# Optimization experiments

Measured on AMD Instinct MI355X. Metric: run time of the kernel, lower is better.

The kernel has to match this reference:

```python
import jax, jax.numpy as jnp
import numpy as np

N_NODES = 100000


def _gcn_conv(x, edge_index, W, b, n_nodes):
    """PyG GCNConv: add self-loops, symmetric deg^-1/2 normalization,
    linear transform, scatter-sum aggregation, bias."""
    loop = jnp.arange(n_nodes, dtype=edge_index.dtype)
    src = jnp.concatenate([edge_index[0], loop])  # message sources
    dst = jnp.concatenate([edge_index[1], loop])  # message targets
    deg = jax.ops.segment_sum(jnp.ones_like(dst, dtype=x.dtype), dst,
                              num_segments=n_nodes)
    dinv = jnp.where(deg > 0, jax.lax.rsqrt(jnp.maximum(deg, 1.0)), 0.0)
    norm = dinv[src] * dinv[dst]  # [E+N]
    h = x @ W  # [N, out] transform before aggregation (fewer bytes moved)
    msg = h[src] * norm[:, None]  # [E+N, out]
    out = jax.ops.segment_sum(msg, dst, num_segments=n_nodes)
    return out + b


def setup_inputs() -> dict:
    key = jax.random.key(0)
    k1, k2, k3, k4, k5, k6 = jax.random.split(key, 6)
    in_ch, hid, out_ch = 128, 64, 64
    x = jax.random.normal(k1, (N_NODES, in_ch), dtype=jnp.float32)
    edge_index = jax.random.randint(k2, (2, 3200000), 0, N_NODES, dtype=jnp.int64)
    # Glorot-style init for GCN weights, zeros for bias (PyG default)
    W1 = jax.random.normal(k3, (in_ch, hid), dtype=jnp.float32) / np.sqrt(in_ch)
    b1 = jnp.zeros((hid,), dtype=jnp.float32)
    W2 = jax.random.normal(k4, (hid, out_ch), dtype=jnp.float32) / np.sqrt(hid)
    b2 = jnp.zeros((out_ch,), dtype=jnp.float32)
    return {"x": x, "edge_index": edge_index, "W1": W1, "b1": b1,
            "W2": W2, "b2": b2}


def reference(x, edge_index, W1, b1, W2, b2):
    n = x.shape[0]
    h = _gcn_conv(x, edge_index, W1, b1, n)
    h = jax.nn.relu(h)
    out = _gcn_conv(h, edge_index, W2, b2, n)
    return out
```

## Files before the change

kernel.cpp:

```cpp
#include <hip/hip_runtime.h>
#include <math.h>


#define BKT_SHIFT 9
#define BKT_NODES 512
#define NBSH      256
#define CHUNK     8192
#define MAXB      20480

typedef unsigned short ushort_t;

static __device__ __forceinline__ unsigned short f2bf(float f) {
    unsigned u = __float_as_uint(f);
    unsigned r = (u + 0x7FFFu + ((u >> 16) & 1u)) >> 16;
    return (unsigned short)r;
}
static __device__ __forceinline__ float bf_lo(unsigned u) {
    return __uint_as_float(u << 16);
}
static __device__ __forceinline__ float bf_hi(unsigned u) {
    return __uint_as_float(u & 0xFFFF0000u);
}

struct ushort4_t { unsigned short x, y, z, w; };

__global__ __launch_bounds__(256) void bucket_bin(const int* __restrict__ src,
                                                  const int* __restrict__ dst,
                                                  int* __restrict__ bcur,
                                                  unsigned* __restrict__ pairs,
                                                  int E, int NB) {
    __shared__ unsigned stag[CHUNK];
    __shared__ int hist[NBSH];
    __shared__ int lofs[NBSH];
    __shared__ int lcur[NBSH];
    __shared__ int gbase[NBSH];
    const int t  = threadIdx.x;
    const int e0 = blockIdx.x * CHUNK;
    const int n  = min(CHUNK, E - e0);

    for (int i = t; i < NBSH; i += 256) hist[i] = 0;
    __syncthreads();
    for (int i = t; i < n; i += 256) atomicAdd(&hist[dst[e0 + i] >> BKT_SHIFT], 1);
    __syncthreads();
    int v = hist[t];
    lofs[t] = v;
    __syncthreads();
    for (int d = 1; d < 256; d <<= 1) {
        int u = (t >= d) ? lofs[t - d] : 0;
        __syncthreads();
        lofs[t] += u;
        __syncthreads();
    }
    if (t < NB) {
        lcur[t]  = lofs[t] - v;
        gbase[t] = (v > 0) ? t * MAXB + atomicAdd(&bcur[t], v) : 0;
    }
    __syncthreads();
    for (int i = t; i < n; i += 256) {
        int d = dst[e0 + i];
        int s = src[e0 + i];
        int b = d >> BKT_SHIFT;
        int p = atomicAdd(&lcur[b], 1);
        stag[p] = ((unsigned)(d & (BKT_NODES - 1)) << 17) | (unsigned)s;
    }
    __syncthreads();
    const int wv = t >> 6, ln = t & 63;
    for (int b = wv; b < NB; b += 4) {
        int cb = hist[b];
        if (cb == 0) continue;
        int lo = lofs[b] - cb;
        int gb = gbase[b];
        int lim = min(cb, (b + 1) * MAXB - gb);
        for (int i = ln; i < lim; i += 64) pairs[gb + i] = stag[lo + i];
    }
}

__global__ __launch_bounds__(1024) void csr_sort(const unsigned* __restrict__ pairs,
                                                 const int* __restrict__ bcur,
                                                 unsigned* __restrict__ csr,
                                                 int* __restrict__ cnt,
                                                 int* __restrict__ offs,
                                                 float* __restrict__ dinv, int N) {
    extern __shared__ unsigned st[];
    __shared__ int h[BKT_NODES];
    __shared__ int sc[BKT_NODES];
    __shared__ int cur[BKT_NODES];
    const int b    = blockIdx.x;
    const int t    = threadIdx.x;
    const int n0   = b << BKT_SHIFT;
    const int base = b * MAXB;
    const int ne   = min(bcur[b], MAXB);

    if (t < BKT_NODES) h[t] = 0;
    __syncthreads();
    for (int i = t; i < ne; i += 1024) atomicAdd(&h[pairs[base + i] >> 17], 1);
    __syncthreads();
    int v = 0;
    if (t < BKT_NODES) { v = h[t]; sc[t] = v; }
    __syncthreads();
    for (int d = 1; d < BKT_NODES; d <<= 1) {
        int u = (t < BKT_NODES && t >= d) ? sc[t - d] : 0;
        __syncthreads();
        if (t < BKT_NODES) sc[t] += u;
        __syncthreads();
    }
    if (t < BKT_NODES) {
        int ex = sc[t] - v;
        cur[t] = ex;
        int node = n0 + t;
        if (node < N) {
            cnt[node]  = v;
            offs[node] = base + ex;
            dinv[node] = rsqrtf((float)(v + 1));
        }
    }
    __syncthreads();
    for (int i = t; i < ne; i += 1024) {
        unsigned p = pairs[base + i];
        int pos = atomicAdd(&cur[p >> 17], 1);
        st[pos] = p & 0x1FFFFu;
    }
    __syncthreads();
    for (int i = t; i < ne; i += 1024) csr[base + i] = st[i];
}

template <int K>
__global__ __launch_bounds__(256) void gemm_scale(const float* __restrict__ X,
                                                  const float* __restrict__ W,
                                                  const float* __restrict__ dinv,
                                                  ushort_t* __restrict__ G, int N) {
    __shared__ float Ws[K * 64];
    const int t  = threadIdx.x;
    const int r0 = blockIdx.x * 128;

    for (int i = t; i < K * 16; i += 256)
        ((float4*)Ws)[i] = ((const float4*)W)[i];

    const int cg = (t & 15) * 4;
    const int rb = r0 + (t >> 4) * 8;

    float acc[8][4];
#pragma unroll
    for (int j = 0; j < 8; ++j) {
        acc[j][0] = 0.f; acc[j][1] = 0.f; acc[j][2] = 0.f; acc[j][3] = 0.f;
    }
    __syncthreads();

    const bool full = (rb + 8 <= N);
    for (int k = 0; k < K; k += 4) {
        float4 xr[8];
        if (full) {
#pragma unroll
            for (int j = 0; j < 8; ++j)
                xr[j] = *(const float4*)(X + (size_t)(rb + j) * K + k);
        } else {
#pragma unroll
            for (int j = 0; j < 8; ++j)
                xr[j] = (rb + j < N) ? *(const float4*)(X + (size_t)(rb + j) * K + k)
                                     : make_float4(0.f, 0.f, 0.f, 0.f);
        }
#pragma unroll
        for (int kk = 0; kk < 4; ++kk) {
            float4 w = *(const float4*)&Ws[(k + kk) * 64 + cg];
#pragma unroll
            for (int j = 0; j < 8; ++j) {
                float xv = (&xr[j].x)[kk];
                acc[j][0] = fmaf(xv, w.x, acc[j][0]);
                acc[j][1] = fmaf(xv, w.y, acc[j][1]);
                acc[j][2] = fmaf(xv, w.z, acc[j][2]);
                acc[j][3] = fmaf(xv, w.w, acc[j][3]);
            }
        }
    }

#pragma unroll
    for (int j = 0; j < 8; ++j) {
        int row = rb + j;
        if (row < N) {
            float s = dinv[row];
            ushort4_t o = { f2bf(acc[j][0] * s), f2bf(acc[j][1] * s),
                            f2bf(acc[j][2] * s), f2bf(acc[j][3] * s) };
            *(ushort4_t*)(G + (size_t)row * 64 + cg) = o;
        }
    }
}

#define ACC8(v)                                         \
    acc[0] += bf_lo((v).x); acc[1] += bf_hi((v).x);     \
    acc[2] += bf_lo((v).y); acc[3] += bf_hi((v).y);     \
    acc[4] += bf_lo((v).z); acc[5] += bf_hi((v).z);     \
    acc[6] += bf_lo((v).w); acc[7] += bf_hi((v).w);

__global__ __launch_bounds__(256) void aggregate5(const ushort_t* __restrict__ G,
                                                  const int* __restrict__ offs,
                                                  const int* __restrict__ cnt,
                                                  const unsigned* __restrict__ csr,
                                                  const float* __restrict__ dinv,
                                                  const float* __restrict__ bias,
                                                  float* __restrict__ out, int N,
                                                  int do_relu) {
    int w    = (blockIdx.x * 256 + threadIdx.x) >> 6;
    int lane = threadIdx.x & 63;
    if (w >= N) return;
    const int grp = lane >> 3;
    const int sub = lane & 7;
    const int beg = offs[w];
    const int num = cnt[w];

    float acc[8] = {0.f, 0.f, 0.f, 0.f, 0.f, 0.f, 0.f, 0.f};
    if (grp == 0) {
        uint4 v = *(const uint4*)(G + (size_t)w * 64 + sub * 8);
        ACC8(v);
    }

    int e = 0;
    for (; e + 32 <= num; e += 32) {
        unsigned s0 = csr[beg + e + grp];
        unsigned s1 = csr[beg + e + 8 + grp];
        unsigned s2 = csr[beg + e + 16 + grp];
        unsigned s3 = csr[beg + e + 24 + grp];
        uint4 v0 = *(const uint4*)(G + ((size_t)s0 << 6) + (sub << 3));
        uint4 v1 = *(const uint4*)(G + ((size_t)s1 << 6) + (sub << 3));
        uint4 v2 = *(const uint4*)(G + ((size_t)s2 << 6) + (sub << 3));
        uint4 v3 = *(const uint4*)(G + ((size_t)s3 << 6) + (sub << 3));
        ACC8(v0); ACC8(v1); ACC8(v2); ACC8(v3);
    }
    if (e + 16 <= num) {
        unsigned s0 = csr[beg + e + grp];
        unsigned s1 = csr[beg + e + 8 + grp];
        uint4 v0 = *(const uint4*)(G + ((size_t)s0 << 6) + (sub << 3));
        uint4 v1 = *(const uint4*)(G + ((size_t)s1 << 6) + (sub << 3));
        ACC8(v0); ACC8(v1);
        e += 16;
    }
    if (e + 8 <= num) {
        unsigned s0 = csr[beg + e + grp];
        uint4 v0 = *(const uint4*)(G + ((size_t)s0 << 6) + (sub << 3));
        ACC8(v0);
        e += 8;
    }
    int rem = num - e;
    if (grp < rem) {
        unsigned s0 = csr[beg + e + grp];
        uint4 v0 = *(const uint4*)(G + ((size_t)s0 << 6) + (sub << 3));
        ACC8(v0);
    }

#pragma unroll
    for (int m = 8; m <= 32; m <<= 1) {
#pragma unroll
        for (int j = 0; j < 8; ++j) acc[j] += __shfl_xor(acc[j], m, 64);
    }

    if (grp == 0) {
        float d = dinv[w];
        float4 bl0 = *(const float4*)(bias + sub * 8);
        float4 bl1 = *(const float4*)(bias + sub * 8 + 4);
        float4 o0 = make_float4(fmaf(acc[0], d, bl0.x), fmaf(acc[1], d, bl0.y),
                                fmaf(acc[2], d, bl0.z), fmaf(acc[3], d, bl0.w));
        float4 o1 = make_float4(fmaf(acc[4], d, bl1.x), fmaf(acc[5], d, bl1.y),
                                fmaf(acc[6], d, bl1.z), fmaf(acc[7], d, bl1.w));
        if (do_relu) {
            o0.x = fmaxf(o0.x, 0.f); o0.y = fmaxf(o0.y, 0.f);
            o0.z = fmaxf(o0.z, 0.f); o0.w = fmaxf(o0.w, 0.f);
            o1.x = fmaxf(o1.x, 0.f); o1.y = fmaxf(o1.y, 0.f);
            o1.z = fmaxf(o1.z, 0.f); o1.w = fmaxf(o1.w, 0.f);
        }
        *(float4*)(out + (size_t)w * 64 + sub * 8)     = o0;
        *(float4*)(out + (size_t)w * 64 + sub * 8 + 4) = o1;
    }
}

extern "C" void kernel_launch(void* const* d_in, const int* in_sizes, int n_in,
                              void* d_out, int out_size, void* d_ws, size_t ws_size,
                              hipStream_t stream) {
    const float* x  = (const float*)d_in[0];
    const int*   ei = (const int*)d_in[1];
    const float* W1 = (const float*)d_in[2];
    const float* b1 = (const float*)d_in[3];
    const float* W2 = (const float*)d_in[4];
    const float* b2 = (const float*)d_in[5];
    float* out = (float*)d_out;

    const int IN_CH = 128;
    const int N = in_sizes[0] / IN_CH;
    const int E = in_sizes[1] / 2;
    const int* src = ei;
    const int* dst = ei + E;
    const int NB = (N + BKT_NODES - 1) >> BKT_SHIFT;

    char* ws = (char*)d_ws;
    size_t off = 0;
    auto take = [&](size_t bytes) -> char* {
        char* p = ws + off;
        off += (bytes + 255) & ~(size_t)255;
        return p;
    };
    float*    dinv  = (float*)take((size_t)N * 4);
    int*      cnt   = (int*)take((size_t)N * 4);
    int*      offs  = (int*)take((size_t)N * 4);
    int*      bcur  = (int*)take(NBSH * 4);
    unsigned* csr   = (unsigned*)take((size_t)NB * MAXB * 4);
    ushort_t* g     = (ushort_t*)take((size_t)N * 64 * 2);
    float*    a1    = (float*)take((size_t)N * 64 * 4);
    unsigned* pairs = (unsigned*)a1;

    const int nbC = (E + CHUNK - 1) / CHUNK;

    hipMemsetAsync(bcur, 0, NBSH * 4, stream);
    bucket_bin<<<nbC, 256, 0, stream>>>(src, dst, bcur, pairs, E, NB);
    csr_sort<<<NB, 1024, MAXB * 4, stream>>>(pairs, bcur, csr, cnt, offs, dinv, N);

    gemm_scale<128><<<(N + 127) / 128, 256, 0, stream>>>(x, W1, dinv, g, N);
    aggregate5<<<(N + 3) / 4, 256, 0, stream>>>(g, offs, cnt, csr, dinv, b1, a1, N, 1);
    gemm_scale<64><<<(N + 127) / 128, 256, 0, stream>>>(a1, W2, dinv, g, N);
    aggregate5<<<(N + 3) / 4, 256, 0, stream>>>(g, offs, cnt, csr, dinv, b2, out, N, 0);
}
```

Baseline: 332.5 us.

## Sort each node's neighbors into source-range slices and aggregate in lockstep phases

The CSR sort now splits each destination's neighbor list into four sub-lists keyed by source-index range (about 25K nodes each) and stores the four lengths packed into a uint2 per node. The aggregation kernel assigns each 8-lane group two destination nodes and walks the four source slices in order, with a block barrier between slices. The goal is that blocks running concurrently gather from the same quarter of G at the same time, which should improve L2 locality. In exchange it adds masked dummy loads for unequal list lengths, per-slice barriers, and 16-bit length limits.

```diff
diff --git a/kernel.cpp b/kernel.cpp
--- a/kernel.cpp
+++ b/kernel.cpp
@@ -75,50 +75,64 @@
     }
 }
 
-__global__ __launch_bounds__(1024) void csr_sort(const unsigned* __restrict__ pairs,
-                                                 const int* __restrict__ bcur,
-                                                 unsigned* __restrict__ csr,
-                                                 int* __restrict__ cnt,
-                                                 int* __restrict__ offs,
-                                                 float* __restrict__ dinv, int N) {
+__global__ __launch_bounds__(1024) void csr_sort3(const unsigned* __restrict__ pairs,
+                                                  const int* __restrict__ bcur,
+                                                  unsigned* __restrict__ csr,
+                                                  int* __restrict__ offs,
+                                                  uint2* __restrict__ cnt4,
+                                                  float* __restrict__ dinv, int N) {
     extern __shared__ unsigned st[];
-    __shared__ int h[BKT_NODES];
-    __shared__ int sc[BKT_NODES];
-    __shared__ int cur[BKT_NODES];
+    __shared__ int h[2048];
+    __shared__ int sc[1024];
     const int b    = blockIdx.x;
     const int t    = threadIdx.x;
     const int n0   = b << BKT_SHIFT;
     const int base = b * MAXB;
     const int ne   = min(bcur[b], MAXB);
 
-    if (t < BKT_NODES) h[t] = 0;
-    __syncthreads();
-    for (int i = t; i < ne; i += 1024) atomicAdd(&h[pairs[base + i] >> 17], 1);
-    __syncthreads();
-    int v = 0;
-    if (t < BKT_NODES) { v = h[t]; sc[t] = v; }
-    __syncthreads();
-    for (int d = 1; d < BKT_NODES; d <<= 1) {
-        int u = (t < BKT_NODES && t >= d) ? sc[t - d] : 0;
-        __syncthreads();
-        if (t < BKT_NODES) sc[t] += u;
-        __syncthreads();
-    }
+    h[t] = 0; h[t + 1024] = 0;
+    __syncthreads();
+    for (int i = t; i < ne; i += 1024) {
+        unsigned p  = pairs[base + i];
+        unsigned sv = p & 0x1FFFFu;
+        int key = (int)(((p >> 17) << 2) | ((sv * 41u) >> 20));
+        atomicAdd(&h[key], 1);
+    }
+    __syncthreads();
     if (t < BKT_NODES) {
-        int ex = sc[t] - v;
-        cur[t] = ex;
         int node = n0 + t;
         if (node < N) {
-            cnt[node]  = v;
-            offs[node] = base + ex;
-            dinv[node] = rsqrtf((float)(v + 1));
-        }
+            int a = h[4 * t], bb = h[4 * t + 1], c = h[4 * t + 2], d = h[4 * t + 3];
+            cnt4[node] = make_uint2((unsigned)a | ((unsigned)bb << 16),
+                                    (unsigned)c | ((unsigned)d << 16));
+            dinv[node] = rsqrtf((float)(a + bb + c + d + 1));
+        }
+    }
+    int v0 = h[2 * t], v1 = h[2 * t + 1];
+    int lsum = v0 + v1;
+    sc[t] = lsum;
+    __syncthreads();
+    for (int d = 1; d < 1024; d <<= 1) {
+        int u = (t >= d) ? sc[t - d] : 0;
+        __syncthreads();
+        sc[t] += u;
+        __syncthreads();
+    }
+    int run = sc[t] - lsum;
+    h[2 * t]     = run;
+    h[2 * t + 1] = run + v0;
+    __syncthreads();
+    if (t < BKT_NODES) {
+        int node = n0 + t;
+        if (node < N) offs[node] = base + h[4 * t];
     }
     __syncthreads();
     for (int i = t; i < ne; i += 1024) {
-        unsigned p = pairs[base + i];
-        int pos = atomicAdd(&cur[p >> 17], 1);
-        st[pos] = p & 0x1FFFFu;
+        unsigned p  = pairs[base + i];
+        unsigned sv = p & 0x1FFFFu;
+        int key = (int)(((p >> 17) << 2) | ((sv * 41u) >> 20));
+        int pos = atomicAdd(&h[key], 1);
+        st[pos] = sv;
     }
     __syncthreads();
     for (int i = t; i < ne; i += 1024) csr[base + i] = st[i];
@@ -185,89 +199,109 @@
     }
 }
 
-#define ACC8(v)                                         \
-    acc[0] += bf_lo((v).x); acc[1] += bf_hi((v).x);     \
-    acc[2] += bf_lo((v).y); acc[3] += bf_hi((v).y);     \
-    acc[4] += bf_lo((v).z); acc[5] += bf_hi((v).z);     \
-    acc[6] += bf_lo((v).w); acc[7] += bf_hi((v).w);
-
-__global__ __launch_bounds__(256) void aggregate5(const ushort_t* __restrict__ G,
+#define ACCA(v)                                           \
+    acc0[0] += bf_lo((v).x); acc0[1] += bf_hi((v).x);     \
+    acc0[2] += bf_lo((v).y); acc0[3] += bf_hi((v).y);     \
+    acc0[4] += bf_lo((v).z); acc0[5] += bf_hi((v).z);     \
+    acc0[6] += bf_lo((v).w); acc0[7] += bf_hi((v).w);
+#define ACCB(v)                                           \
+    acc1[0] += bf_lo((v).x); acc1[1] += bf_hi((v).x);     \
+    acc1[2] += bf_lo((v).y); acc1[3] += bf_hi((v).y);     \
+    acc1[4] += bf_lo((v).z); acc1[5] += bf_hi((v).z);     \
+    acc1[6] += bf_lo((v).w); acc1[7] += bf_hi((v).w);
+
+__global__ __launch_bounds__(256) void aggregate7(const ushort_t* __restrict__ G,
                                                   const int* __restrict__ offs,
-                                                  const int* __restrict__ cnt,
+                                                  const uint2* __restrict__ cnt4,
                                                   const unsigned* __restrict__ csr,
                                                   const float* __restrict__ dinv,
                                                   const float* __restrict__ bias,
                                                   float* __restrict__ out, int N,
                                                   int do_relu) {
-    int w    = (blockIdx.x * 256 + threadIdx.x) >> 6;
-    int lane = threadIdx.x & 63;
-    if (w >= N) return;
-    const int grp = lane >> 3;
-    const int sub = lane & 7;
-    const int beg = offs[w];
-    const int num = cnt[w];
-
-    float acc[8] = {0.f, 0.f, 0.f, 0.f, 0.f, 0.f, 0.f, 0.f};
-    if (grp == 0) {
-        uint4 v = *(const uint4*)(G + (size_t)w * 64 + sub * 8);
-        ACC8(v);
-    }
-
-    int e = 0;
-    for (; e + 32 <= num; e += 32) {
-        unsigned s0 = csr[beg + e + grp];
-        unsigned s1 = csr[beg + e + 8 + grp];
-        unsigned s2 = csr[beg + e + 16 + grp];
-        unsigned s3 = csr[beg + e + 24 + grp];
-        uint4 v0 = *(const uint4*)(G + ((size_t)s0 << 6) + (sub << 3));
-        uint4 v1 = *(const uint4*)(G + ((size_t)s1 << 6) + (sub << 3));
-        uint4 v2 = *(const uint4*)(G + ((size_t)s2 << 6) + (sub << 3));
-        uint4 v3 = *(const uint4*)(G + ((size_t)s3 << 6) + (sub << 3));
-        ACC8(v0); ACC8(v1); ACC8(v2); ACC8(v3);
-    }
-    if (e + 16 <= num) {
-        unsigned s0 = csr[beg + e + grp];
-        unsigned s1 = csr[beg + e + 8 + grp];
-        uint4 v0 = *(const uint4*)(G + ((size_t)s0 << 6) + (sub << 3));
-        uint4 v1 = *(const uint4*)(G + ((size_t)s1 << 6) + (sub << 3));
-        ACC8(v0); ACC8(v1);
-        e += 16;
-    }
-    if (e + 8 <= num) {
-        unsigned s0 = csr[beg + e + grp];
-        uint4 v0 = *(const uint4*)(G + ((size_t)s0 << 6) + (sub << 3));
-        ACC8(v0);
-        e += 8;
-    }
-    int rem = num - e;
-    if (grp < rem) {
-        unsigned s0 = csr[beg + e + grp];
-        uint4 v0 = *(const uint4*)(G + ((size_t)s0 << 6) + (sub << 3));
-        ACC8(v0);
-    }
-
-#pragma unroll
-    for (int m = 8; m <= 32; m <<= 1) {
-#pragma unroll
-        for (int j = 0; j < 8; ++j) acc[j] += __shfl_xor(acc[j], m, 64);
-    }
-
-    if (grp == 0) {
-        float d = dinv[w];
-        float4 bl0 = *(const float4*)(bias + sub * 8);
-        float4 bl1 = *(const float4*)(bias + sub * 8 + 4);
-        float4 o0 = make_float4(fmaf(acc[0], d, bl0.x), fmaf(acc[1], d, bl0.y),
-                                fmaf(acc[2], d, bl0.z), fmaf(acc[3], d, bl0.w));
-        float4 o1 = make_float4(fmaf(acc[4], d, bl1.x), fmaf(acc[5], d, bl1.y),
-                                fmaf(acc[6], d, bl1.z), fmaf(acc[7], d, bl1.w));
+    const int t   = threadIdx.x;
+    const int sub = t & 7;
+    const int gg  = t >> 3;
+    const int nA  = blockIdx.x * 64 + gg * 2;
+    const int nB  = nA + 1;
+
+    const bool okA = (nA < N), okB = (nB < N);
+    uint2 cA = okA ? cnt4[nA] : make_uint2(0u, 0u);
+    uint2 cB = okB ? cnt4[nB] : make_uint2(0u, 0u);
+    int posA = okA ? offs[nA] : 0;
+    int posB = okB ? offs[nB] : 0;
+
+    float acc0[8] = {0.f, 0.f, 0.f, 0.f, 0.f, 0.f, 0.f, 0.f};
+    float acc1[8] = {0.f, 0.f, 0.f, 0.f, 0.f, 0.f, 0.f, 0.f};
+
+#pragma unroll
+    for (int s = 0; s < 4; ++s) {
+        const int lenA = (int)((s == 0 ? cA.x : s == 1 ? cA.x >> 16
+                              : s == 2 ? cA.y : cA.y >> 16) & 0xFFFFu);
+        const int lenB = (int)((s == 0 ? cB.x : s == 1 ? cB.x >> 16
+                              : s == 2 ? cB.y : cB.y >> 16) & 0xFFFFu);
+        const int jm = max(lenA, lenB);
+        for (int j = 0; j < jm; j += 2) {
+            const int j1 = j + 1;
+            const bool aA0 = j < lenA, aA1 = j1 < lenA;
+            const bool aB0 = j < lenB, aB1 = j1 < lenB;
+            unsigned sA0 = csr[posA + (aA0 ? j : 0)];
+            unsigned sB0 = csr[posB + (aB0 ? j : 0)];
+            unsigned sA1 = csr[posA + (aA1 ? j1 : 0)];
+            unsigned sB1 = csr[posB + (aB1 ? j1 : 0)];
+            uint4 vA0 = *(const uint4*)(G + ((size_t)sA0 << 6) + (sub << 3));
+            uint4 vB0 = *(const uint4*)(G + ((size_t)sB0 << 6) + (sub << 3));
+            uint4 vA1 = *(const uint4*)(G + ((size_t)sA1 << 6) + (sub << 3));
+            uint4 vB1 = *(const uint4*)(G + ((size_t)sB1 << 6) + (sub << 3));
+            unsigned mA0 = aA0 ? 0xFFFFFFFFu : 0u;
+            unsigned mB0 = aB0 ? 0xFFFFFFFFu : 0u;
+            unsigned mA1 = aA1 ? 0xFFFFFFFFu : 0u;
+            unsigned mB1 = aB1 ? 0xFFFFFFFFu : 0u;
+            vA0.x &= mA0; vA0.y &= mA0; vA0.z &= mA0; vA0.w &= mA0;
+            vB0.x &= mB0; vB0.y &= mB0; vB0.z &= mB0; vB0.w &= mB0;
+            vA1.x &= mA1; vA1.y &= mA1; vA1.z &= mA1; vA1.w &= mA1;
+            vB1.x &= mB1; vB1.y &= mB1; vB1.z &= mB1; vB1.w &= mB1;
+            ACCA(vA0); ACCB(vB0); ACCA(vA1); ACCB(vB1);
+        }
+        posA += lenA;
+        posB += lenB;
+        __syncthreads();
+    }
+
+    float4 bl0 = *(const float4*)(bias + sub * 8);
+    float4 bl1 = *(const float4*)(bias + sub * 8 + 4);
+    if (okA) {
+        uint4 v = *(const uint4*)(G + ((size_t)nA << 6) + (sub << 3));
+        ACCA(v);
+        float d = dinv[nA];
+        float4 o0 = make_float4(fmaf(acc0[0], d, bl0.x), fmaf(acc0[1], d, bl0.y),
+                                fmaf(acc0[2], d, bl0.z), fmaf(acc0[3], d, bl0.w));
+        float4 o1 = make_float4(fmaf(acc0[4], d, bl1.x), fmaf(acc0[5], d, bl1.y),
+                                fmaf(acc0[6], d, bl1.z), fmaf(acc0[7], d, bl1.w));
         if (do_relu) {
             o0.x = fmaxf(o0.x, 0.f); o0.y = fmaxf(o0.y, 0.f);
             o0.z = fmaxf(o0.z, 0.f); o0.w = fmaxf(o0.w, 0.f);
             o1.x = fmaxf(o1.x, 0.f); o1.y = fmaxf(o1.y, 0.f);
             o1.z = fmaxf(o1.z, 0.f); o1.w = fmaxf(o1.w, 0.f);
         }
-        *(float4*)(out + (size_t)w * 64 + sub * 8)     = o0;
-        *(float4*)(out + (size_t)w * 64 + sub * 8 + 4) = o1;
+        *(float4*)(out + (size_t)nA * 64 + sub * 8)     = o0;
+        *(float4*)(out + (size_t)nA * 64 + sub * 8 + 4) = o1;
+    }
+    if (okB) {
+        uint4 v = *(const uint4*)(G + ((size_t)nB << 6) + (sub << 3));
+        ACCB(v);
+        float d = dinv[nB];
+        float4 o0 = make_float4(fmaf(acc1[0], d, bl0.x), fmaf(acc1[1], d, bl0.y),
+                                fmaf(acc1[2], d, bl0.z), fmaf(acc1[3], d, bl0.w));
+        float4 o1 = make_float4(fmaf(acc1[4], d, bl1.x), fmaf(acc1[5], d, bl1.y),
+                                fmaf(acc1[6], d, bl1.z), fmaf(acc1[7], d, bl1.w));
+        if (do_relu) {
+            o0.x = fmaxf(o0.x, 0.f); o0.y = fmaxf(o0.y, 0.f);
+            o0.z = fmaxf(o0.z, 0.f); o0.w = fmaxf(o0.w, 0.f);
+            o1.x = fmaxf(o1.x, 0.f); o1.y = fmaxf(o1.y, 0.f);
+            o1.z = fmaxf(o1.z, 0.f); o1.w = fmaxf(o1.w, 0.f);
+        }
+        *(float4*)(out + (size_t)nB * 64 + sub * 8)     = o0;
+        *(float4*)(out + (size_t)nB * 64 + sub * 8 + 4) = o1;
     }
 }
 
@@ -297,22 +331,23 @@
         return p;
     };
     float*    dinv  = (float*)take((size_t)N * 4);
-    int*      cnt   = (int*)take((size_t)N * 4);
     int*      offs  = (int*)take((size_t)N * 4);
+    uint2*    cnt4  = (uint2*)take((size_t)N * 8);
     int*      bcur  = (int*)take(NBSH * 4);
-    unsigned* csr   = (unsigned*)take((size_t)NB * MAXB * 4);
+    unsigned* csr   = (unsigned*)take(((size_t)NB * MAXB + 64) * 4);
     ushort_t* g     = (ushort_t*)take((size_t)N * 64 * 2);
     float*    a1    = (float*)take((size_t)N * 64 * 4);
     unsigned* pairs = (unsigned*)a1;
 
     const int nbC = (E + CHUNK - 1) / CHUNK;
+    const int nbA = (N + 63) / 64;
 
     hipMemsetAsync(bcur, 0, NBSH * 4, stream);
     bucket_bin<<<nbC, 256, 0, stream>>>(src, dst, bcur, pairs, E, NB);
-    csr_sort<<<NB, 1024, MAXB * 4, stream>>>(pairs, bcur, csr, cnt, offs, dinv, N);
+    csr_sort3<<<NB, 1024, MAXB * 4, stream>>>(pairs, bcur, csr, offs, cnt4, dinv, N);
 
     gemm_scale<128><<<(N + 127) / 128, 256, 0, stream>>>(x, W1, dinv, g, N);
-    aggregate5<<<(N + 3) / 4, 256, 0, stream>>>(g, offs, cnt, csr, dinv, b1, a1, N, 1);
+    aggregate7<<<nbA, 256, 0, stream>>>(g, offs, cnt4, csr, dinv, b1, a1, N, 1);
     gemm_scale<64><<<(N + 127) / 128, 256, 0, stream>>>(a1, W2, dinv, g, N);
-    aggregate5<<<(N + 3) / 4, 256, 0, stream>>>(g, offs, cnt, csr, dinv, b2, out, N, 0);
-}
+    aggregate7<<<nbA, 256, 0, stream>>>(g, offs, cnt4, csr, dinv, b2, out, N, 0);
+}
```

Result: no change. 334.2 us (+0.5%).
